# Performance work log

Hardware: AMD Instinct MI355X
Metric: run time of the kernel (lower is better)

The kernel has to match this reference:

```python
import jax, jax.numpy as jnp
import numpy as np

B, L, D = 2, 2048, 2048
H = 16
DH = D // H  # 128
EPS = 1e-6


def _rope_cos_sin(seq_len, dim, dtype):
    inv_freq = 1.0 / (10000.0 ** (jnp.arange(0, dim, 2, dtype=jnp.float32) / dim))
    t = jnp.arange(seq_len, dtype=jnp.float32)
    freqs = jnp.einsum('i,j->ij', t, inv_freq)          # [L, dim/2]
    emb = jnp.concatenate([freqs, freqs], axis=-1)      # [L, dim]
    return jnp.cos(emb).astype(dtype)[None, None], jnp.sin(emb).astype(dtype)[None, None]


def _rotate_half(x):
    x1, x2 = jnp.split(x, 2, axis=-1)
    return jnp.concatenate([-x2, x1], axis=-1)


def _rms_norm(x, w):
    var = jnp.mean(jnp.square(x), axis=-1, keepdims=True)
    return x * jax.lax.rsqrt(var + EPS) * w


def setup_inputs() -> dict:
    key = jax.random.key(0)
    ks = jax.random.split(key, 4)
    s_in = 1.0 / np.sqrt(D)
    return {
        'x': jax.random.normal(ks[0], (B, L, D), jnp.float32),
        'attention_mask': jnp.zeros((B, 1, 1, L), jnp.bool_),
        'Wqkv': jax.random.normal(ks[1], (D, 3 * D), jnp.float32) * s_in,
        'bqkv': jnp.zeros((3 * D,), jnp.float32),
        'Wout': jax.random.normal(ks[2], (D, D), jnp.float32) * s_in,
        'bout': jnp.zeros((D,), jnp.float32),
        'q_norm_w': jnp.ones((DH,), jnp.float32),
        'k_norm_w': jnp.ones((DH,), jnp.float32),
    }


def reference(x, attention_mask, Wqkv, bqkv, Wout, bout, q_norm_w, k_norm_w):
    b, l, d = x.shape
    qkv = x @ Wqkv + bqkv                                   # [B,L,3D]
    q, k, v = jnp.split(qkv, 3, axis=-1)
    # [B,H,L,DH]
    q = q.reshape(b, l, H, DH).transpose(0, 2, 1, 3)
    k = k.reshape(b, l, H, DH).transpose(0, 2, 1, 3)
    v = v.reshape(b, l, H, DH).transpose(0, 2, 1, 3)

    cos, sin = _rope_cos_sin(l, DH, x.dtype)
    q = q * cos + _rotate_half(q) * sin
    k = k * cos + _rotate_half(k) * sin

    q = _rms_norm(q, q_norm_w)
    k = _rms_norm(k, k_norm_w)

    # SDPA with additive (float-cast) mask, as in the original code
    scale = 1.0 / np.sqrt(DH)
    scores = jnp.einsum('bhqd,bhkd->bhqk', q, k) * scale
    scores = scores + attention_mask.astype(x.dtype)        # broadcast [B,1,1,L]
    attn = jax.nn.softmax(scores, axis=-1)
    out = jnp.einsum('bhqk,bhkd->bhqd', attn, v)            # [B,H,L,DH]

    # zero out masked query rows: padding_mask = mask.transpose(2,3) -> [B,1,L,1]
    padding_mask = jnp.swapaxes(attention_mask, 2, 3)
    out = jnp.where(padding_mask, 0.0, out)

    out = out.transpose(0, 2, 1, 3).reshape(b, l, d)
    return out @ Wout + bout
```

## Files before the change

### kernel.cpp

```cpp
#include <hip/hip_runtime.h>
#include <hip/hip_bf16.h>

typedef __bf16 bf16;
using bf16x8 = __attribute__((ext_vector_type(8))) __bf16;
using bf16x4 = __attribute__((ext_vector_type(4))) __bf16;
using f32x4  = __attribute__((ext_vector_type(4))) float;
using f32x16 = __attribute__((ext_vector_type(16))) float;

#define DEV __device__ __forceinline__

DEV void load_lds16(const void* g, void* l) {
  __builtin_amdgcn_global_load_lds(
      (const __attribute__((address_space(1))) void*)g,
      (__attribute__((address_space(3))) void*)l, 16, 0, 0);
}

__global__ void k_tab(float* __restrict__ ct, float* __restrict__ st) {
  int l = blockIdx.x, i = threadIdx.x;
  double invf = pow(10000.0, -(double)i / 64.0);
  double a = (double)l * invf;
  ct[l * 64 + i] = (float)cos(a);
  st[l * 64 + i] = (float)sin(a);
}

__global__ void k_f2b(const float* __restrict__ in, bf16* __restrict__ out, long n) {
  long i = ((long)blockIdx.x * blockDim.x + threadIdx.x) * 8;
  if (i >= n) return;
  float4 a = *(const float4*)(in + i);
  float4 b = *(const float4*)(in + i + 4);
  bf16x8 o;
  o[0] = (bf16)a.x; o[1] = (bf16)a.y; o[2] = (bf16)a.z; o[3] = (bf16)a.w;
  o[4] = (bf16)b.x; o[5] = (bf16)b.y; o[6] = (bf16)b.z; o[7] = (bf16)b.w;
  *(bf16x8*)(out + i) = o;
}

__global__ __launch_bounds__(256) void k_tconv(const float* __restrict__ in,
                                               bf16* __restrict__ out, int R, int C) {
  __shared__ float t[64][65];
  int nbc = C >> 6;
  long r0 = (long)(blockIdx.x / nbc) * 64, c0 = (long)(blockIdx.x % nbc) * 64;
  int tid = threadIdx.x;
#pragma unroll
  for (int i = 0; i < 4; ++i) {
    int ch = tid + i * 256;
    int r = ch >> 4, c4 = (ch & 15) * 4;
    float4 v = *(const float4*)(in + (r0 + r) * C + c0 + c4);
    t[r][c4] = v.x; t[r][c4 + 1] = v.y; t[r][c4 + 2] = v.z; t[r][c4 + 3] = v.w;
  }
  __syncthreads();
#pragma unroll
  for (int i = 0; i < 2; ++i) {
    int ch = tid + i * 256;
    int c = ch >> 3, r8 = (ch & 7) * 8;
    bf16x8 o;
#pragma unroll
    for (int j = 0; j < 8; ++j) o[j] = (bf16)t[r8 + j][c];
    *(bf16x8*)(out + (c0 + c) * R + r0 + r8) = o;
  }
}

template <typename OutT>
__global__ __launch_bounds__(256) void k_gemm_bt(
    const bf16* __restrict__ A, const bf16* __restrict__ Bt,
    const float* __restrict__ bias, OutT* __restrict__ C,
    int M, int N, int K) {
  __shared__ __align__(16) bf16 lA[128 * 64];
  __shared__ __align__(16) bf16 lB[128 * 64];
  int bid = blockIdx.x;
  if ((gridDim.x & 7) == 0) {
    int q = gridDim.x >> 3;
    bid = (bid & 7) * q + (bid >> 3);
  }
  int nbn = N >> 7;
  int bm = bid / nbn, bn = bid % nbn;
  const int tid = threadIdx.x, lane = tid & 63, wid = tid >> 6;
  const int wr = wid >> 1, wc = wid & 1;
  const int fr = lane & 15, fq = lane >> 4;
  const long abase = (long)bm * 128 * K, bbase = (long)bn * 128 * K;
  f32x4 acc[4][4] = {};

  for (int k0 = 0; k0 < K; k0 += 64) {
    __syncthreads();
#pragma unroll
    for (int it = 0; it < 4; ++it) {
      int ch = it * 256 + tid;
      int r = ch >> 3, u = ch & 7;
      load_lds16(A + abase + (long)r * K + k0 + ((u ^ (r & 7)) << 3), &lA[ch * 8]);
    }
#pragma unroll
    for (int it = 0; it < 4; ++it) {
      int ch = it * 256 + tid;
      int r = ch >> 3, u = ch & 7;
      load_lds16(Bt + bbase + (long)r * K + k0 + ((u ^ (r & 7)) << 3), &lB[ch * 8]);
    }
    __syncthreads();
    bf16x8 af[4][2], bf_[4][2];
#pragma unroll
    for (int m = 0; m < 4; ++m) {
      int R = wr * 64 + m * 16 + fr;
#pragma unroll
      for (int kk = 0; kk < 2; ++kk)
        af[m][kk] = *(const bf16x8*)&lA[R * 64 + (((kk * 4 + fq) ^ (R & 7)) << 3)];
    }
#pragma unroll
    for (int n = 0; n < 4; ++n) {
      int R = wc * 64 + n * 16 + fr;
#pragma unroll
      for (int kk = 0; kk < 2; ++kk)
        bf_[n][kk] = *(const bf16x8*)&lB[R * 64 + (((kk * 4 + fq) ^ (R & 7)) << 3)];
    }
#pragma unroll
    for (int m = 0; m < 4; ++m)
#pragma unroll
      for (int n = 0; n < 4; ++n)
#pragma unroll
        for (int kk = 0; kk < 2; ++kk)
          acc[m][n] = __builtin_amdgcn_mfma_f32_16x16x32_bf16(af[m][kk], bf_[n][kk],
                                                              acc[m][n], 0, 0, 0);
  }
#pragma unroll
  for (int n = 0; n < 4; ++n) {
    int col = bn * 128 + wc * 64 + n * 16 + fr;
    float bv = bias[col];
#pragma unroll
    for (int m = 0; m < 4; ++m) {
      int row0 = bm * 128 + wr * 64 + m * 16 + fq * 4;
#pragma unroll
      for (int r = 0; r < 4; ++r) {
        float v = acc[m][n][r] + bv;
        C[(long)(row0 + r) * N + col] = (OutT)v;
      }
    }
  }
}

__global__ __launch_bounds__(256) void k_qkpost(
    const bf16* __restrict__ qkv, const float* __restrict__ ct, const float* __restrict__ st,
    const float* __restrict__ qw, const float* __restrict__ kw,
    bf16* __restrict__ q_r, bf16* __restrict__ k_r) {
  int bl = blockIdx.x;
  int l = bl & 2047;
  int b = bl >> 11;
  int tid = threadIdx.x;
  int h = tid >> 4, i8 = (tid & 15) * 8;
  bool lo = i8 < 64;
  float c[8], s[8];
#pragma unroll
  for (int j = 0; j < 8; ++j) {
    int d = (i8 + j) & 63;
    c[j] = ct[l * 64 + d];
    s[j] = st[l * 64 + d];
  }
#pragma unroll
  for (int part = 0; part < 2; ++part) {
    bf16x8 xv = *(const bf16x8*)(qkv + (long)bl * 6144 + part * 2048 + h * 128 + i8);
    float v[8], p[8], r[8];
    float ss = 0.f;
#pragma unroll
    for (int j = 0; j < 8; ++j) v[j] = (float)xv[j];
#pragma unroll
    for (int j = 0; j < 8; ++j) p[j] = __shfl_xor(v[j], 8);
#pragma unroll
    for (int j = 0; j < 8; ++j) {
      r[j] = lo ? v[j] * c[j] - p[j] * s[j] : v[j] * c[j] + p[j] * s[j];
      ss += r[j] * r[j];
    }
    ss += __shfl_xor(ss, 1);
    ss += __shfl_xor(ss, 2);
    ss += __shfl_xor(ss, 4);
    ss += __shfl_xor(ss, 8);
    float inv = rsqrtf(ss * (1.f / 128.f) + 1e-6f);
    const float* wv = part ? kw : qw;
    bf16* dst = (part ? k_r : q_r) + ((long)(b * 16 + h) * 2048 + l) * 128 + i8;
    bf16x8 ov;
#pragma unroll
    for (int j = 0; j < 8; ++j) ov[j] = (bf16)(r[j] * inv * wv[i8 + j]);
    *(bf16x8*)dst = ov;
  }
}

__global__ __launch_bounds__(256) void k_vt(const bf16* __restrict__ qkv, bf16* __restrict__ v_t) {
  __shared__ bf16 t[64][130];
  int blk = blockIdx.x;
  int lt = blk & 31, bh = blk >> 5;
  int b = bh >> 4, h = bh & 15;
  int l0 = lt * 64;
  int tid = threadIdx.x;
#pragma unroll
  for (int i = 0; i < 4; ++i) {
    int ch = tid + i * 256;
    int r = ch >> 4, c8 = (ch & 15) * 8;
    bf16x8 v = *(const bf16x8*)(qkv + (long)(b * 2048 + l0 + r) * 6144 + 4096 + h * 128 + c8);
#pragma unroll
    for (int j = 0; j < 8; ++j) t[r][c8 + j] = v[j];
  }
  __syncthreads();
#pragma unroll
  for (int i = 0; i < 4; ++i) {
    int ch = tid + i * 256;
    int d = ch >> 3, l8 = (ch & 7) * 8;
    bf16x8 o;
#pragma unroll
    for (int j = 0; j < 8; ++j) o[j] = t[l8 + j][d];
    *(bf16x8*)(v_t + ((long)bh * 128 + d) * 2048 + l0 + l8) = o;
  }
}

__global__ __launch_bounds__(512, 2) void k_attn(
    const bf16* __restrict__ q_r, const bf16* __restrict__ k_r,
    const bf16* __restrict__ v_t, const unsigned char* __restrict__ amask,
    bf16* __restrict__ attno) {
  __shared__ __align__(16) bf16 lK[2][64 * 128];
  __shared__ __align__(16) bf16 lV[2][128 * 64];
  __shared__ int sAny;
  const int tid = threadIdx.x, lane = tid & 63, w = tid >> 6;
  const int hi = lane >> 5, q31 = lane & 31;
  const int qt = blockIdx.x & 7, bh = blockIdx.x >> 3;
  const int b = bh >> 4, h = bh & 15;
  const long hbase = (long)bh * 2048 * 128;
  const int q0 = qt * 256 + w * 32;
  const unsigned char* mb = amask + b * 2048;

  if (tid == 0) sAny = 0;
  __syncthreads();
  {
    unsigned mv = *(const unsigned*)(mb + tid * 4);
    if (mv) sAny = 1;
  }

  bf16x8 qf[8];
#pragma unroll
  for (int ksl = 0; ksl < 8; ++ksl)
    qf[ksl] = *(const bf16x8*)(q_r + hbase + (long)(q0 + q31) * 128 + ksl * 16 + hi * 8);

  f32x16 o[4] = {};
  float m_run = -1e30f, l_run = 0.f;
  const float SC2 = 0.08838834764831845f * 1.4426950408889634f;
  const float L2E = 1.4426950408889634f;

#define STAGE(buf, kv0)                                                              \
  {                                                                                  \
    _Pragma("unroll") for (int it = 0; it < 2; ++it) {                               \
      int g = it * 512 + w * 64 + lane;                                              \
      int r = g >> 4, u = g & 15;                                                    \
      load_lds16(k_r + hbase + (long)((kv0) + r) * 128 + ((u ^ (r & 7)) << 3),       \
                 &lK[buf][(it * 512 + w * 64) * 8]);                                 \
    }                                                                                \
    _Pragma("unroll") for (int it = 0; it < 2; ++it) {                               \
      int g = it * 512 + w * 64 + lane;                                              \
      int r = g >> 3, u = g & 7;                                                     \
      load_lds16(v_t + hbase + (long)r * 2048 + (kv0) + ((u ^ (r & 7)) << 3),        \
                 &lV[buf][(it * 512 + w * 64) * 8]);                                 \
    }                                                                                \
  }

  STAGE(0, 0);
  __syncthreads();
  const bool maskAny = sAny != 0;
  int cur = 0;
  for (int t = 0; t < 32; ++t) {
    const int kv0 = t << 6;
    if (t < 31) STAGE(cur ^ 1, kv0 + 64);

    f32x16 st0 = {}, st1 = {};
#pragma unroll
    for (int ksl = 0; ksl < 8; ++ksl) {
      const int u = ksl * 2 + hi;
      bf16x8 kf0 = *(const bf16x8*)&lK[cur][q31 * 128 + ((u ^ (q31 & 7)) << 3)];
      bf16x8 kf1 = *(const bf16x8*)&lK[cur][(32 + q31) * 128 + ((u ^ (q31 & 7)) << 3)];
      st0 = __builtin_amdgcn_mfma_f32_32x32x16_bf16(kf0, qf[ksl], st0, 0, 0, 0);
      st1 = __builtin_amdgcn_mfma_f32_32x32x16_bf16(kf1, qf[ksl], st1, 0, 0, 0);
    }

#pragma unroll
    for (int i = 0; i < 16; ++i) { st0[i] *= SC2; st1[i] *= SC2; }
    if (maskAny) {
#pragma unroll
      for (int i = 0; i < 16; ++i) {
        int c = (i & 3) + 8 * (i >> 2) + 4 * hi;
        if (mb[kv0 + c]) st0[i] += L2E;
        if (mb[kv0 + 32 + c]) st1[i] += L2E;
      }
    }

    float tm = st0[0];
#pragma unroll
    for (int i = 1; i < 16; ++i) tm = fmaxf(tm, st0[i]);
#pragma unroll
    for (int i = 0; i < 16; ++i) tm = fmaxf(tm, st1[i]);
    tm = fmaxf(tm, __shfl_xor(tm, 32));

    if (!__all(tm <= m_run + 8.f)) {
      float mn = fmaxf(m_run, tm);
      float corr = exp2f(m_run - mn);
      m_run = mn;
      l_run *= corr;
#pragma unroll
      for (int i = 0; i < 16; ++i) {
        float cr = __shfl(corr, (i & 3) + 8 * (i >> 2) + 4 * hi);
#pragma unroll
        for (int dt = 0; dt < 4; ++dt) o[dt][i] *= cr;
      }
    }

    float rs = 0.f;
#pragma unroll
    for (int i = 0; i < 16; ++i) { st0[i] = exp2f(st0[i] - m_run); rs += st0[i]; }
#pragma unroll
    for (int i = 0; i < 16; ++i) { st1[i] = exp2f(st1[i] - m_run); rs += st1[i]; }
    rs += __shfl_xor(rs, 32);
    l_run += rs;

    union UU { bf16x4 v; uint2 u; };
    union U8 { bf16x8 v; uint4 u; };
    bf16x8 pa[4];
#define MKPA(pidx, STX, bb)                                                          \
  {                                                                                  \
    UU plo, phi;                                                                     \
    plo.v = (bf16x4){(bf16)STX[bb], (bf16)STX[(bb) + 1], (bf16)STX[(bb) + 2],        \
                     (bf16)STX[(bb) + 3]};                                           \
    phi.v = (bf16x4){(bf16)STX[(bb) + 4], (bf16)STX[(bb) + 5], (bf16)STX[(bb) + 6],  \
                     (bf16)STX[(bb) + 7]};                                           \
    unsigned sx = hi ? plo.u.x : phi.u.x, sy = hi ? plo.u.y : phi.u.y;               \
    unsigned rx = (unsigned)__shfl_xor((int)sx, 32), ry = (unsigned)__shfl_xor((int)sy, 32); \
    U8 f;                                                                            \
    f.u.x = hi ? rx : plo.u.x; f.u.y = hi ? ry : plo.u.y;                            \
    f.u.z = hi ? phi.u.x : rx; f.u.w = hi ? phi.u.y : ry;                            \
    pa[pidx] = f.v;                                                                  \
  }
    MKPA(0, st0, 0) MKPA(1, st0, 8) MKPA(2, st1, 0) MKPA(3, st1, 8)
#undef MKPA

#pragma unroll
    for (int dt = 0; dt < 4; ++dt) {
      const int dr = dt * 32 + q31;
#pragma unroll
      for (int ks = 0; ks < 4; ++ks) {
        const int u = ks * 2 + hi;
        bf16x8 vb = *(const bf16x8*)&lV[cur][dr * 64 + ((u ^ (dr & 7)) << 3)];
        o[dt] = __builtin_amdgcn_mfma_f32_32x32x16_bf16(pa[ks], vb, o[dt], 0, 0, 0);
      }
    }

    __syncthreads();
    cur ^= 1;
  }
#undef STAGE

  float invl = 1.f / l_run;
#pragma unroll
  for (int i = 0; i < 16; ++i) {
    int q = (i & 3) + 8 * (i >> 2) + 4 * hi;
    int qrow = q0 + q;
    float inv = __shfl(invl, q);
    float zm = inv;
    if (maskAny) { if (mb[qrow]) zm = 0.f; }
#pragma unroll
    for (int dt = 0; dt < 4; ++dt)
      attno[(long)(b * 2048 + qrow) * 2048 + h * 128 + dt * 32 + q31] = (bf16)(o[dt][i] * zm);
  }
}

extern "C" void kernel_launch(void* const* d_in, const int* in_sizes, int n_in,
                              void* d_out, int out_size, void* d_ws, size_t ws_size,
                              hipStream_t stream) {
  const float* x = (const float*)d_in[0];
  const unsigned char* amask = (const unsigned char*)d_in[1];
  const float* Wqkv = (const float*)d_in[2];
  const float* bqkv = (const float*)d_in[3];
  const float* Wout = (const float*)d_in[4];
  const float* bout = (const float*)d_in[5];
  const float* qw = (const float*)d_in[6];
  const float* kw = (const float*)d_in[7];
  float* out = (float*)d_out;
  char* ws = (char*)d_ws;

  bf16* xb   = (bf16*)(ws);
  bf16* wqT  = (bf16*)(ws + 16777216);
  bf16* woT  = (bf16*)(ws + 41943040);
  bf16* qkv  = (bf16*)(ws + 50331648);
  bf16* q_r  = (bf16*)(ws + 100663296);
  bf16* k_r  = (bf16*)(ws + 117440512);
  bf16* v_t  = (bf16*)(ws + 134217728);
  float* ct  = (float*)(ws + 150994944);
  float* st  = ct + 2048 * 64;
  bf16* attno = xb;

  k_tab<<<2048, 64, 0, stream>>>(ct, st);
  k_f2b<<<4096, 256, 0, stream>>>(x, xb, 8388608L);
  k_tconv<<<32 * 96, 256, 0, stream>>>(Wqkv, wqT, 2048, 6144);
  k_tconv<<<32 * 32, 256, 0, stream>>>(Wout, woT, 2048, 2048);
  k_gemm_bt<bf16><<<32 * 48, 256, 0, stream>>>(xb, wqT, bqkv, qkv, 4096, 6144, 2048);
  k_qkpost<<<4096, 256, 0, stream>>>(qkv, ct, st, qw, kw, q_r, k_r);
  k_vt<<<1024, 256, 0, stream>>>(qkv, v_t);
  k_attn<<<256, 512, 0, stream>>>(q_r, k_r, v_t, amask, attno);
  k_gemm_bt<float><<<32 * 16, 256, 0, stream>>>(attno, woT, bout, out, 4096, 2048, 2048);
}
```

Baseline: 329.8 us.

## Fuse RoPE, RMSNorm and V transpose into the QKV GEMM epilogue

The QKV GEMM epilogue now stages each 128x128 output tile in LDS and applies RoPE plus RMSNorm for the Q and K column blocks, or transposes the V block, writing q_r, k_r and v_t directly. This removes the bf16 qkv intermediate round-trip through global memory and two separate kernel launches. In exchange the GEMM gains a longer epilogue with extra syncs, more register pressure from the runtime fuse branch, and cos/sin table reads per row.

```diff
diff --git a/kernel.cpp b/kernel.cpp
--- a/kernel.cpp
+++ b/kernel.cpp
@@ -63,9 +63,13 @@
 __global__ __launch_bounds__(256) void k_gemm_bt(
     const bf16* __restrict__ A, const bf16* __restrict__ Bt,
     const float* __restrict__ bias, OutT* __restrict__ C,
-    int M, int N, int K) {
-  __shared__ __align__(16) bf16 lA[128 * 64];
-  __shared__ __align__(16) bf16 lB[128 * 64];
+    int M, int N, int K, int fuse,
+    const float* __restrict__ ct, const float* __restrict__ st,
+    const float* __restrict__ qw, const float* __restrict__ kw,
+    bf16* __restrict__ q_r, bf16* __restrict__ k_r, bf16* __restrict__ v_t) {
+  __shared__ __align__(16) bf16 lAB[2][128 * 64];
+  bf16* lA = lAB[0];
+  bf16* lB = lAB[1];
   int bid = blockIdx.x;
   if ((gridDim.x & 7) == 0) {
     int q = gridDim.x >> 3;
@@ -118,91 +122,106 @@
           acc[m][n] = __builtin_amdgcn_mfma_f32_16x16x32_bf16(af[m][kk], bf_[n][kk],
                                                               acc[m][n], 0, 0, 0);
   }
-#pragma unroll
-  for (int n = 0; n < 4; ++n) {
-    int col = bn * 128 + wc * 64 + n * 16 + fr;
-    float bv = bias[col];
-#pragma unroll
-    for (int m = 0; m < 4; ++m) {
-      int row0 = bm * 128 + wr * 64 + m * 16 + fq * 4;
-#pragma unroll
-      for (int r = 0; r < 4; ++r) {
-        float v = acc[m][n][r] + bv;
-        C[(long)(row0 + r) * N + col] = (OutT)v;
-      }
-    }
-  }
-}
-
-__global__ __launch_bounds__(256) void k_qkpost(
-    const bf16* __restrict__ qkv, const float* __restrict__ ct, const float* __restrict__ st,
-    const float* __restrict__ qw, const float* __restrict__ kw,
-    bf16* __restrict__ q_r, bf16* __restrict__ k_r) {
-  int bl = blockIdx.x;
-  int l = bl & 2047;
-  int b = bl >> 11;
-  int tid = threadIdx.x;
-  int h = tid >> 4, i8 = (tid & 15) * 8;
-  bool lo = i8 < 64;
-  float c[8], s[8];
-#pragma unroll
-  for (int j = 0; j < 8; ++j) {
-    int d = (i8 + j) & 63;
-    c[j] = ct[l * 64 + d];
-    s[j] = st[l * 64 + d];
-  }
-#pragma unroll
-  for (int part = 0; part < 2; ++part) {
-    bf16x8 xv = *(const bf16x8*)(qkv + (long)bl * 6144 + part * 2048 + h * 128 + i8);
-    float v[8], p[8], r[8];
-    float ss = 0.f;
-#pragma unroll
-    for (int j = 0; j < 8; ++j) v[j] = (float)xv[j];
-#pragma unroll
-    for (int j = 0; j < 8; ++j) p[j] = __shfl_xor(v[j], 8);
-#pragma unroll
-    for (int j = 0; j < 8; ++j) {
-      r[j] = lo ? v[j] * c[j] - p[j] * s[j] : v[j] * c[j] + p[j] * s[j];
-      ss += r[j] * r[j];
-    }
-    ss += __shfl_xor(ss, 1);
-    ss += __shfl_xor(ss, 2);
-    ss += __shfl_xor(ss, 4);
-    ss += __shfl_xor(ss, 8);
-    float inv = rsqrtf(ss * (1.f / 128.f) + 1e-6f);
-    const float* wv = part ? kw : qw;
-    bf16* dst = (part ? k_r : q_r) + ((long)(b * 16 + h) * 2048 + l) * 128 + i8;
-    bf16x8 ov;
-#pragma unroll
-    for (int j = 0; j < 8; ++j) ov[j] = (bf16)(r[j] * inv * wv[i8 + j]);
-    *(bf16x8*)dst = ov;
-  }
-}
-
-__global__ __launch_bounds__(256) void k_vt(const bf16* __restrict__ qkv, bf16* __restrict__ v_t) {
-  __shared__ bf16 t[64][130];
-  int blk = blockIdx.x;
-  int lt = blk & 31, bh = blk >> 5;
-  int b = bh >> 4, h = bh & 15;
-  int l0 = lt * 64;
-  int tid = threadIdx.x;
-#pragma unroll
-  for (int i = 0; i < 4; ++i) {
-    int ch = tid + i * 256;
-    int r = ch >> 4, c8 = (ch & 15) * 8;
-    bf16x8 v = *(const bf16x8*)(qkv + (long)(b * 2048 + l0 + r) * 6144 + 4096 + h * 128 + c8);
-#pragma unroll
-    for (int j = 0; j < 8; ++j) t[r][c8 + j] = v[j];
-  }
+
+  if (!fuse) {
+#pragma unroll
+    for (int n = 0; n < 4; ++n) {
+      int col = bn * 128 + wc * 64 + n * 16 + fr;
+      float bv = bias[col];
+#pragma unroll
+      for (int m = 0; m < 4; ++m) {
+        int row0 = bm * 128 + wr * 64 + m * 16 + fq * 4;
+#pragma unroll
+        for (int r = 0; r < 4; ++r) {
+          float v = acc[m][n][r] + bv;
+          C[(long)(row0 + r) * N + col] = (OutT)v;
+        }
+      }
+    }
+    return;
+  }
+
   __syncthreads();
-#pragma unroll
-  for (int i = 0; i < 4; ++i) {
-    int ch = tid + i * 256;
-    int d = ch >> 3, l8 = (ch & 7) * 8;
-    bf16x8 o;
-#pragma unroll
-    for (int j = 0; j < 8; ++j) o[j] = t[l8 + j][d];
-    *(bf16x8*)(v_t + ((long)bh * 128 + d) * 2048 + l0 + l8) = o;
+  bf16* tile = lAB[0];
+  const int h = bn & 15;
+  const int b = bm >> 4, l0 = (bm & 15) << 7;
+
+  if (bn < 32) {
+#pragma unroll
+    for (int n = 0; n < 4; ++n) {
+      int col = wc * 64 + n * 16 + fr;
+      float bv = bias[bn * 128 + col];
+#pragma unroll
+      for (int m = 0; m < 4; ++m)
+#pragma unroll
+        for (int r = 0; r < 4; ++r) {
+          int row = wr * 64 + m * 16 + fq * 4 + r;
+          tile[row * 128 + (col ^ ((row & 7) << 3))] = (bf16)(acc[m][n][r] + bv);
+        }
+    }
+    __syncthreads();
+    const float* wv = (bn < 16) ? qw : kw;
+    bf16* dst0 = (bn < 16) ? q_r : k_r;
+    const int tcol = tid & 15, rgrp = tid >> 4, i8 = tcol * 8;
+    const bool lo = i8 < 64;
+    float wvv[8];
+#pragma unroll
+    for (int j = 0; j < 8; ++j) wvv[j] = wv[i8 + j];
+#pragma unroll
+    for (int it = 0; it < 8; ++it) {
+      int row = it * 16 + rgrp;
+      int l = l0 + row;
+      float cc[8], sn[8];
+#pragma unroll
+      for (int j = 0; j < 8; ++j) {
+        int d = (i8 + j) & 63;
+        cc[j] = ct[l * 64 + d];
+        sn[j] = st[l * 64 + d];
+      }
+      bf16x8 xv = *(const bf16x8*)&tile[row * 128 + (i8 ^ ((row & 7) << 3))];
+      float v[8], p[8], rr[8];
+      float ss = 0.f;
+#pragma unroll
+      for (int j = 0; j < 8; ++j) v[j] = (float)xv[j];
+#pragma unroll
+      for (int j = 0; j < 8; ++j) p[j] = __shfl_xor(v[j], 8);
+#pragma unroll
+      for (int j = 0; j < 8; ++j) {
+        rr[j] = lo ? v[j] * cc[j] - p[j] * sn[j] : v[j] * cc[j] + p[j] * sn[j];
+        ss += rr[j] * rr[j];
+      }
+      ss += __shfl_xor(ss, 1);
+      ss += __shfl_xor(ss, 2);
+      ss += __shfl_xor(ss, 4);
+      ss += __shfl_xor(ss, 8);
+      float inv = rsqrtf(ss * (1.f / 128.f) + 1e-6f);
+      bf16x8 ov;
+#pragma unroll
+      for (int j = 0; j < 8; ++j) ov[j] = (bf16)(rr[j] * inv * wvv[j]);
+      *(bf16x8*)(dst0 + ((long)((b * 16 + h) * 2048 + l)) * 128 + i8) = ov;
+    }
+  } else {
+#pragma unroll
+    for (int n = 0; n < 4; ++n) {
+      int col = wc * 64 + n * 16 + fr;
+      float bv = bias[bn * 128 + col];
+#pragma unroll
+      for (int m = 0; m < 4; ++m)
+#pragma unroll
+        for (int r = 0; r < 4; ++r) {
+          int row = wr * 64 + m * 16 + fq * 4 + r;
+          tile[col * 128 + (row ^ ((col & 7) << 3))] = (bf16)(acc[m][n][r] + bv);
+        }
+    }
+    __syncthreads();
+    const int d = tid >> 1, lh = (tid & 1) << 6;
+    bf16* dst = v_t + ((long)((b * 16 + h) * 128 + d)) * 2048 + l0 + lh;
+#pragma unroll
+    for (int k2 = 0; k2 < 8; ++k2) {
+      int l8 = lh + k2 * 8;
+      bf16x8 vv = *(const bf16x8*)&tile[d * 128 + (l8 ^ ((d & 7) << 3))];
+      *(bf16x8*)(dst + k2 * 8) = vv;
+    }
   }
 }
 
@@ -378,7 +397,6 @@
   bf16* xb   = (bf16*)(ws);
   bf16* wqT  = (bf16*)(ws + 16777216);
   bf16* woT  = (bf16*)(ws + 41943040);
-  bf16* qkv  = (bf16*)(ws + 50331648);
   bf16* q_r  = (bf16*)(ws + 100663296);
   bf16* k_r  = (bf16*)(ws + 117440512);
   bf16* v_t  = (bf16*)(ws + 134217728);
@@ -390,9 +408,12 @@
   k_f2b<<<4096, 256, 0, stream>>>(x, xb, 8388608L);
   k_tconv<<<32 * 96, 256, 0, stream>>>(Wqkv, wqT, 2048, 6144);
   k_tconv<<<32 * 32, 256, 0, stream>>>(Wout, woT, 2048, 2048);
-  k_gemm_bt<bf16><<<32 * 48, 256, 0, stream>>>(xb, wqT, bqkv, qkv, 4096, 6144, 2048);
-  k_qkpost<<<4096, 256, 0, stream>>>(qkv, ct, st, qw, kw, q_r, k_r);
-  k_vt<<<1024, 256, 0, stream>>>(qkv, v_t);
+  k_gemm_bt<bf16><<<32 * 48, 256, 0, stream>>>(xb, wqT, bqkv, (bf16*)nullptr,
+                                               4096, 6144, 2048, 1,
+                                               ct, st, qw, kw, q_r, k_r, v_t);
   k_attn<<<256, 512, 0, stream>>>(q_r, k_r, v_t, amask, attno);
-  k_gemm_bt<float><<<32 * 16, 256, 0, stream>>>(attno, woT, bout, out, 4096, 2048, 2048);
-}
+  k_gemm_bt<float><<<32 * 16, 256, 0, stream>>>(attno, woT, bout, out,
+                                                4096, 2048, 2048, 0,
+                                                nullptr, nullptr, nullptr, nullptr,
+                                                nullptr, nullptr, nullptr);
+}
```

New measurement: 314.1 us. 4.8% less time.
